# Optimization experiments

Measured on AMD Instinct MI355X. Metric: run time of the kernel, lower is better.

Reference implementation:

```python
import jax, jax.numpy as jnp
import numpy as np


def setup_inputs() -> dict:
    key = jax.random.key(0)
    ks = jax.random.split(key, 5)
    b, n_q, n_kv = 16, 128, 4096
    query_dim, context_dim, heads, dim_head = 1024, 1024, 16, 64
    inner = heads * dim_head
    x = jax.random.normal(ks[0], (b, n_q, query_dim), dtype=jnp.float32)
    context = jax.random.normal(ks[1], (b, n_kv, context_dim), dtype=jnp.float32)
    # Linear weights stored as (in, out); scaled like default torch init magnitude
    Wq = jax.random.normal(ks[2], (query_dim, inner), dtype=jnp.float32) * (query_dim ** -0.5)
    Wkv = jax.random.normal(ks[3], (context_dim, 2 * inner), dtype=jnp.float32) * (context_dim ** -0.5)
    Wout = jax.random.normal(ks[4], (inner, query_dim), dtype=jnp.float32) * (inner ** -0.5)
    bout = jnp.zeros((query_dim,), dtype=jnp.float32)
    return {"x": x, "context": context, "Wq": Wq, "Wkv": Wkv, "Wout": Wout, "bout": bout}


def reference(x, context, Wq, Wkv, Wout, bout):
    heads, dim_head = 16, 64
    b, n_q, _ = x.shape
    n_kv = context.shape[1]
    scale = dim_head ** -0.5

    q = x @ Wq                       # [b, n_q, h*d]
    kv = context @ Wkv               # [b, n_kv, 2*h*d]
    k, v = jnp.split(kv, 2, axis=-1)

    def split_heads(t):
        bb, n, _ = t.shape
        return t.reshape(bb, n, heads, dim_head).transpose(0, 2, 1, 3)  # [b, h, n, d]

    q, k, v = map(split_heads, (q, k, v))

    # mask[i, j] = (i - (j % n_q) == 0)  -> query i attends keys j with j % n_q == i
    i_idx = jnp.arange(n_q)[:, None]
    j_idx = jnp.arange(n_kv)[None, :]
    mask = (j_idx % n_q) == i_idx      # [n_q, n_kv] bool

    sim = jnp.einsum('bhid,bhjd->bhij', q, k) * scale
    max_neg = -jnp.finfo(sim.dtype).max
    sim = jnp.where(mask[None, None, :, :], sim, max_neg)
    attn = jax.nn.softmax(sim, axis=-1)
    out = jnp.einsum('bhij,bhjd->bhid', attn, v)   # [b, h, n_q, d]
    out = out.transpose(0, 2, 1, 3).reshape(b, n_q, heads * dim_head)
    return out @ Wout + bout
```

## Files before the change

### kernel.cpp

```cpp
#include <hip/hip_runtime.h>
#include <hip/hip_bf16.h>

typedef __attribute__((ext_vector_type(8))) short short8;
typedef __attribute__((ext_vector_type(4))) float floatx4;

__device__ __forceinline__ unsigned short f32_to_bf16(float f) {
    unsigned int u = __builtin_bit_cast(unsigned int, f);
    u = (u + 0x7FFFu + ((u >> 16) & 1u)) >> 16;
    return (unsigned short)u;
}
__device__ __forceinline__ unsigned int pack_bf16x2(float lo, float hi) {
    return (unsigned int)f32_to_bf16(lo) | ((unsigned int)f32_to_bf16(hi) << 16);
}
__device__ __forceinline__ void async_load16(const unsigned short* g, unsigned short* l) {
    __builtin_amdgcn_global_load_lds(
        (const __attribute__((address_space(1))) void*)g,
        (__attribute__((address_space(3))) void*)l, 16, 0, 0);
}

__device__ __forceinline__ void transpose_tile(
    const float* __restrict__ W, int src_ld, int n_off,
    unsigned short* __restrict__ Wt, int dst_ld, int nb, int kb, int tid) {
    __shared__ float tile[32][33];
    int n0 = nb * 32, k0 = kb * 32;
    int tx = tid & 31, ty = tid >> 5;
#pragma unroll
    for (int p = 0; p < 4; ++p) {
        int r = ty + 8 * p;
        tile[r][tx] = W[(long)(k0 + r) * src_ld + n_off + n0 + tx];
    }
    __syncthreads();
#pragma unroll
    for (int p = 0; p < 4; ++p) {
        int r = ty + 8 * p;
        Wt[(long)(n0 + r) * dst_ld + k0 + tx] = f32_to_bf16(tile[tx][r]);
    }
}

__device__ __forceinline__ void cast8(
    const float* __restrict__ src, unsigned short* __restrict__ dst) {
    float4 a = *(const float4*)src;
    float4 b = *(const float4*)(src + 4);
    uint4 p;
    p.x = pack_bf16x2(a.x, a.y); p.y = pack_bf16x2(a.z, a.w);
    p.z = pack_bf16x2(b.x, b.y); p.w = pack_bf16x2(b.z, b.w);
    *(uint4*)dst = p;
}

__global__ __launch_bounds__(256) void prep_kernel(
    const float* __restrict__ Wq, const float* __restrict__ Wkv,
    const float* __restrict__ Wout, const float* __restrict__ x,
    unsigned short* __restrict__ WqT, unsigned short* __restrict__ WkB,
    unsigned short* __restrict__ WvT, unsigned short* __restrict__ WoutT,
    unsigned short* __restrict__ xb) {
    int id = blockIdx.x, tid = threadIdx.x;
    if (id < 1024) { transpose_tile(Wq,   1024, 0,    WqT,   1024, id & 31, id >> 5, tid); return; }
    id -= 1024;
    if (id < 1024) { transpose_tile(Wkv,  2048, 1024, WvT,   1024, id & 31, id >> 5, tid); return; }
    id -= 1024;
    if (id < 1024) { transpose_tile(Wout, 1024, 0,    WoutT, 1024, id & 31, id >> 5, tid); return; }
    id -= 1024;
    if (id < 512) {
        long e = ((long)id * 256 + tid) * 8;
        long row = e >> 10, col = e & 1023;
        cast8(Wkv + row * 2048 + col, WkB + e);
        return;
    }
    id -= 512;
    { long e = ((long)id * 256 + tid) * 8; cast8(x + e, xb + e); }
}

__global__ __launch_bounds__(256, 2) void gemm_bt_kernel(
    const unsigned short* __restrict__ A, long sA, int lda,
    const unsigned short* __restrict__ Bt, long sB, int ldb,
    void* __restrict__ C, long sC, int ldc,
    const float* __restrict__ bias, int K, int out_bf16) {
    __shared__ unsigned short As[128 * 32];
    __shared__ unsigned short Bs[128 * 32];

    const int tid = threadIdx.x, wave = tid >> 6, lane = tid & 63;
    const int z = blockIdx.z;
    A  += (long)z * sA;
    Bt += (long)z * sB;
    const int m0 = blockIdx.y * 128, n0 = blockIdx.x * 128;
    const int wrow = (wave >> 1) * 64, wcol = (wave & 1) * 64;

    floatx4 acc[4][4];
#pragma unroll
    for (int i = 0; i < 4; ++i)
#pragma unroll
        for (int j = 0; j < 4; ++j) acc[i][j] = (floatx4)0.0f;

    const int srow = wave * 32 + (lane >> 2);
    const int kofs = (lane & 3) * 8;
    const unsigned short* aAddr = A  + (long)(m0 + srow) * lda + kofs;
    const unsigned short* bAddr = Bt + (long)(n0 + srow) * ldb + kofs;
    unsigned short* asBase = &As[wave * 1024];
    unsigned short* bsBase = &Bs[wave * 1024];

    const int frm = lane & 15, fk = (lane >> 4) * 8;

    for (int kk = 0; kk < K; kk += 32) {
        __syncthreads();
        async_load16(aAddr + kk,                  asBase);
        async_load16(aAddr + (long)16 * lda + kk, asBase + 512);
        async_load16(bAddr + kk,                  bsBase);
        async_load16(bAddr + (long)16 * ldb + kk, bsBase + 512);
        __syncthreads();

        short8 afrag[4], bfrag[4];
#pragma unroll
        for (int rt = 0; rt < 4; ++rt)
            afrag[rt] = *(const short8*)&As[(wrow + rt * 16 + frm) * 32 + fk];
#pragma unroll
        for (int ct = 0; ct < 4; ++ct)
            bfrag[ct] = *(const short8*)&Bs[(wcol + ct * 16 + frm) * 32 + fk];
#pragma unroll
        for (int rt = 0; rt < 4; ++rt)
#pragma unroll
            for (int ct = 0; ct < 4; ++ct)
                acc[rt][ct] = __builtin_amdgcn_mfma_f32_16x16x32_bf16(
                    afrag[rt], bfrag[ct], acc[rt][ct], 0, 0, 0);
    }

    const int orow0 = m0 + wrow + (lane >> 4) * 4;
    const int ocol0 = n0 + wcol + (lane & 15);
    if (out_bf16) {
        unsigned short* Cb = (unsigned short*)C + (long)z * sC;
#pragma unroll
        for (int rt = 0; rt < 4; ++rt)
#pragma unroll
            for (int r = 0; r < 4; ++r) {
                long row = orow0 + rt * 16 + r;
#pragma unroll
                for (int ct = 0; ct < 4; ++ct)
                    Cb[row * ldc + ocol0 + ct * 16] = f32_to_bf16(acc[rt][ct][r]);
            }
    } else {
        float* Cf = (float*)C + (long)z * sC;
#pragma unroll
        for (int rt = 0; rt < 4; ++rt)
#pragma unroll
            for (int r = 0; r < 4; ++r) {
                long row = orow0 + rt * 16 + r;
#pragma unroll
                for (int ct = 0; ct < 4; ++ct) {
                    int col = ocol0 + ct * 16;
                    float v = acc[rt][ct][r];
                    if (bias) v += bias[col];
                    Cf[row * ldc + col] = v;
                }
            }
    }
}

__global__ __launch_bounds__(256, 2) void gemm_n64_kernel(
    const unsigned short* __restrict__ A, long sA, int lda,
    const unsigned short* __restrict__ Bt, long sB, int ldb,
    unsigned short* __restrict__ C, long sC, int ldc, int K) {
    __shared__ unsigned short As[256 * 32];
    __shared__ unsigned short Bs[64 * 32];

    const int tid = threadIdx.x, wave = tid >> 6, lane = tid & 63;
    const int z = blockIdx.z;
    A  += (long)z * sA;
    Bt += (long)z * sB;
    C  += (long)z * sC;
    const int m0 = blockIdx.y * 256;

    floatx4 acc[4][4];
#pragma unroll
    for (int i = 0; i < 4; ++i)
#pragma unroll
        for (int j = 0; j < 4; ++j) acc[i][j] = (floatx4)0.0f;

    const int srow = tid >> 2;
    const int kofs = (tid & 3) * 8;
    const unsigned short* aBase = A  + (long)(m0 + srow) * lda + kofs;
    const unsigned short* bAddr = Bt + (long)srow * ldb + kofs;
    unsigned short* asW = &As[wave * 512];
    unsigned short* bsW = &Bs[wave * 512];

    const int frm = lane & 15, fk = (lane >> 4) * 8;

    for (int kk = 0; kk < K; kk += 32) {
        __syncthreads();
        async_load16(aBase + kk,                   asW);
        async_load16(aBase + (long)64  * lda + kk, asW + 2048);
        async_load16(aBase + (long)128 * lda + kk, asW + 4096);
        async_load16(aBase + (long)192 * lda + kk, asW + 6144);
        async_load16(bAddr + kk,                   bsW);
        __syncthreads();

        short8 afrag[4], bfrag[4];
#pragma unroll
        for (int rt = 0; rt < 4; ++rt)
            afrag[rt] = *(const short8*)&As[(wave * 64 + rt * 16 + frm) * 32 + fk];
#pragma unroll
        for (int ct = 0; ct < 4; ++ct)
            bfrag[ct] = *(const short8*)&Bs[(ct * 16 + frm) * 32 + fk];
#pragma unroll
        for (int rt = 0; rt < 4; ++rt)
#pragma unroll
            for (int ct = 0; ct < 4; ++ct)
                acc[rt][ct] = __builtin_amdgcn_mfma_f32_16x16x32_bf16(
                    afrag[rt], bfrag[ct], acc[rt][ct], 0, 0, 0);
    }

    const int orow0 = m0 + wave * 64 + (lane >> 4) * 4;
    const int ocol0 = lane & 15;
#pragma unroll
    for (int rt = 0; rt < 4; ++rt)
#pragma unroll
        for (int r = 0; r < 4; ++r) {
            long row = orow0 + rt * 16 + r;
#pragma unroll
            for (int ct = 0; ct < 4; ++ct)
                C[row * ldc + ocol0 + ct * 16] = f32_to_bf16(acc[rt][ct][r]);
        }
}

#define CLD 1032
__global__ __launch_bounds__(256) void attn_fused_kernel(
    const float* __restrict__ ctx,
    const unsigned short* __restrict__ qt,
    unsigned short* __restrict__ wctx) {
    __shared__ unsigned short ctx_t[32 * CLD];
    __shared__ unsigned short qt_t[16 * CLD];
    __shared__ float sred[4 * 512];
    __shared__ float s_f[512];
    __shared__ float mxs[16], inv_[16];
    __shared__ unsigned short p_l[16 * 40];

    const int tid = threadIdx.x, wave = tid >> 6, lane = tid & 63;
    const int bi = blockIdx.x;
    const int b = bi >> 7, i = bi & 127;
    const int frm = lane & 15, fk = (lane >> 4) * 8;

#pragma unroll
    for (int rr = 0; rr < 8; ++rr) {
        int idx = rr * 2048 + tid * 8;
        int h = idx >> 10, c = idx & 1023;
        *(uint4*)&qt_t[h * CLD + c] =
            *(const uint4*)&qt[(long)h * 2048 * 1024 + (long)bi * 1024 + c];
    }
#pragma unroll
    for (int rr = 0; rr < 16; ++rr) {
        int idx = rr * 2048 + tid * 8;
        int t = idx >> 10, c = idx & 1023;
        cast8(ctx + ((long)b * 4096 + i + t * 128) * 1024 + c, &ctx_t[t * CLD + c]);
    }
    __syncthreads();

    floatx4 acc0 = (floatx4)0.0f, acc1 = (floatx4)0.0f;
#pragma unroll
    for (int it = 0; it < 8; ++it) {
        int kk = wave * 256 + it * 32;
        short8 af = *(const short8*)&qt_t[frm * CLD + kk + fk];
        short8 b0 = *(const short8*)&ctx_t[frm * CLD + kk + fk];
        short8 b1 = *(const short8*)&ctx_t[(16 + frm) * CLD + kk + fk];
        acc0 = __builtin_amdgcn_mfma_f32_16x16x32_bf16(af, b0, acc0, 0, 0, 0);
        acc1 = __builtin_amdgcn_mfma_f32_16x16x32_bf16(af, b1, acc1, 0, 0, 0);
    }
#pragma unroll
    for (int r = 0; r < 4; ++r) {
        sred[wave * 512 + frm * 16 + (lane >> 4) * 4 + r]        = acc0[r];
        sred[wave * 512 + (16 + frm) * 16 + (lane >> 4) * 4 + r] = acc1[r];
    }
    __syncthreads();
#pragma unroll
    for (int half = 0; half < 2; ++half) {
        int idx = half * 256 + tid;
        s_f[idx] = (sred[idx] + sred[512 + idx] + sred[1024 + idx] + sred[1536 + idx]) * 0.125f;
    }
    __syncthreads();
    if (tid < 16) {
        int h = tid;
        float m = -1e30f;
        for (int t = 0; t < 32; ++t) m = fmaxf(m, s_f[t * 16 + h]);
        float den = 0.0f;
        for (int t = 0; t < 32; ++t) den += __expf(s_f[t * 16 + h] - m);
        mxs[h] = m; inv_[h] = 1.0f / den;
    }
    __syncthreads();
#pragma unroll
    for (int half = 0; half < 2; ++half) {
        int idx = half * 256 + tid;
        int t = idx >> 4, h = idx & 15;
        p_l[h * 40 + t] = f32_to_bf16(__expf(s_f[idx] - mxs[h]) * inv_[h]);
    }
    __syncthreads();

    short8 ap;
#pragma unroll
    for (int j = 0; j < 8; ++j) ap[j] = (short)p_l[frm * 40 + fk + j];
#pragma unroll 4
    for (int nt = 0; nt < 16; ++nt) {
        int c0 = wave * 256 + nt * 16;
        short8 bt;
#pragma unroll
        for (int j = 0; j < 8; ++j) bt[j] = (short)ctx_t[(fk + j) * CLD + c0 + frm];
        floatx4 wacc = __builtin_amdgcn_mfma_f32_16x16x32_bf16(ap, bt, (floatx4)0.0f, 0, 0, 0);
#pragma unroll
        for (int r = 0; r < 4; ++r) {
            int h = (lane >> 4) * 4 + r;
            wctx[(long)h * 2048 * 1024 + (long)bi * 1024 + c0 + frm] = f32_to_bf16(wacc[r]);
        }
    }
}

extern "C" void kernel_launch(void* const* d_in, const int* in_sizes, int n_in,
                              void* d_out, int out_size, void* d_ws, size_t ws_size,
                              hipStream_t stream) {
    const float* x       = (const float*)d_in[0];
    const float* context = (const float*)d_in[1];
    const float* Wq      = (const float*)d_in[2];
    const float* Wkv     = (const float*)d_in[3];
    const float* Wout    = (const float*)d_in[4];
    const float* bout    = (const float*)d_in[5];
    float* out = (float*)d_out;

    char* ws = (char*)d_ws;
    unsigned short* WqT   = (unsigned short*)(ws);
    unsigned short* WkB   = (unsigned short*)(ws + (2ll  << 20));
    unsigned short* WvT   = (unsigned short*)(ws + (4ll  << 20));
    unsigned short* WoutT = (unsigned short*)(ws + (6ll  << 20));
    unsigned short* xb    = (unsigned short*)(ws + (8ll  << 20));
    unsigned short* qb    = (unsigned short*)(ws + (12ll << 20));
    unsigned short* aob   = (unsigned short*)(ws + (16ll << 20));
    unsigned short* qtb   = (unsigned short*)(ws + (32ll << 20));
    unsigned short* wctxb = (unsigned short*)(ws + (96ll << 20));

    prep_kernel<<<4608, 256, 0, stream>>>(Wq, Wkv, Wout, x, WqT, WkB, WvT, WoutT, xb);

    gemm_bt_kernel<<<dim3(8, 16, 1), 256, 0, stream>>>(
        xb, 0, 1024, WqT, 0, 1024, qb, 0, 1024, nullptr, 1024, 1);
    gemm_bt_kernel<<<dim3(8, 16, 16), 256, 0, stream>>>(
        qb, 64, 1024, WkB, 64, 1024, qtb, (long)2048 * 1024, 1024, nullptr, 64, 1);
    attn_fused_kernel<<<2048, 256, 0, stream>>>(context, qtb, wctxb);
    gemm_n64_kernel<<<dim3(1, 8, 16), 256, 0, stream>>>(
        wctxb, (long)2048 * 1024, 1024, WvT, (long)64 * 1024, 1024, aob, 64, 1024, 1024);
    gemm_bt_kernel<<<dim3(8, 16, 1), 256, 0, stream>>>(
        aob, 0, 1024, WoutT, 0, 1024, out, 0, 1024, bout, 1024, 0);
}
```

Measured before the change: 501.1 us.

## Use one 128x64 GEMM kernel, batch-major qt/wctx layouts, register-resident Q in attention

Replaces the 128x128 and n64 GEMM kernels with a single 128x64-tile kernel that allows more blocks per CU, and launches twice as many blocks for the small GEMMs. The per-head intermediates qt and wctx move from head-major to batch-major layout so the attention kernel reads and writes contiguous 32KB per row. The attention kernel now loads its Q fragments straight into registers instead of staging them in LDS, which cuts LDS use and lets it declare two blocks per CU. The cost is smaller GEMM tiles with less operand reuse, and more global traffic for B tiles.

Result: faster. 478.9 us (-4.4%).

```diff
diff --git a/kernel.cpp b/kernel.cpp
--- a/kernel.cpp
+++ b/kernel.cpp
@@ -70,33 +70,31 @@
     { long e = ((long)id * 256 + tid) * 8; cast8(x + e, xb + e); }
 }
 
-__global__ __launch_bounds__(256, 2) void gemm_bt_kernel(
+__global__ __launch_bounds__(256, 4) void gemm64_kernel(
     const unsigned short* __restrict__ A, long sA, int lda,
     const unsigned short* __restrict__ Bt, long sB, int ldb,
     void* __restrict__ C, long sC, int ldc,
     const float* __restrict__ bias, int K, int out_bf16) {
     __shared__ unsigned short As[128 * 32];
-    __shared__ unsigned short Bs[128 * 32];
+    __shared__ unsigned short Bs[64 * 32];
 
     const int tid = threadIdx.x, wave = tid >> 6, lane = tid & 63;
     const int z = blockIdx.z;
     A  += (long)z * sA;
     Bt += (long)z * sB;
-    const int m0 = blockIdx.y * 128, n0 = blockIdx.x * 128;
-    const int wrow = (wave >> 1) * 64, wcol = (wave & 1) * 64;
-
-    floatx4 acc[4][4];
-#pragma unroll
-    for (int i = 0; i < 4; ++i)
+    const int m0 = blockIdx.y * 128, n0 = blockIdx.x * 64;
+
+    floatx4 acc[2][4];
+#pragma unroll
+    for (int i = 0; i < 2; ++i)
 #pragma unroll
         for (int j = 0; j < 4; ++j) acc[i][j] = (floatx4)0.0f;
 
-    const int srow = wave * 32 + (lane >> 2);
     const int kofs = (lane & 3) * 8;
-    const unsigned short* aAddr = A  + (long)(m0 + srow) * lda + kofs;
-    const unsigned short* bAddr = Bt + (long)(n0 + srow) * ldb + kofs;
+    const unsigned short* aAddr = A  + (long)(m0 + wave * 32 + (lane >> 2)) * lda + kofs;
+    const unsigned short* bAddr = Bt + (long)(n0 + wave * 16 + (lane >> 2)) * ldb + kofs;
     unsigned short* asBase = &As[wave * 1024];
-    unsigned short* bsBase = &Bs[wave * 1024];
+    unsigned short* bsBase = &Bs[wave * 512];
 
     const int frm = lane & 15, fk = (lane >> 4) * 8;
 
@@ -105,30 +103,29 @@
         async_load16(aAddr + kk,                  asBase);
         async_load16(aAddr + (long)16 * lda + kk, asBase + 512);
         async_load16(bAddr + kk,                  bsBase);
-        async_load16(bAddr + (long)16 * ldb + kk, bsBase + 512);
         __syncthreads();
 
-        short8 afrag[4], bfrag[4];
-#pragma unroll
-        for (int rt = 0; rt < 4; ++rt)
-            afrag[rt] = *(const short8*)&As[(wrow + rt * 16 + frm) * 32 + fk];
+        short8 afrag[2], bfrag[4];
+#pragma unroll
+        for (int rt = 0; rt < 2; ++rt)
+            afrag[rt] = *(const short8*)&As[(wave * 32 + rt * 16 + frm) * 32 + fk];
 #pragma unroll
         for (int ct = 0; ct < 4; ++ct)
-            bfrag[ct] = *(const short8*)&Bs[(wcol + ct * 16 + frm) * 32 + fk];
-#pragma unroll
-        for (int rt = 0; rt < 4; ++rt)
+            bfrag[ct] = *(const short8*)&Bs[(ct * 16 + frm) * 32 + fk];
+#pragma unroll
+        for (int rt = 0; rt < 2; ++rt)
 #pragma unroll
             for (int ct = 0; ct < 4; ++ct)
                 acc[rt][ct] = __builtin_amdgcn_mfma_f32_16x16x32_bf16(
                     afrag[rt], bfrag[ct], acc[rt][ct], 0, 0, 0);
     }
 
-    const int orow0 = m0 + wrow + (lane >> 4) * 4;
-    const int ocol0 = n0 + wcol + (lane & 15);
+    const int orow0 = m0 + wave * 32 + (lane >> 4) * 4;
+    const int ocol0 = n0 + (lane & 15);
     if (out_bf16) {
         unsigned short* Cb = (unsigned short*)C + (long)z * sC;
 #pragma unroll
-        for (int rt = 0; rt < 4; ++rt)
+        for (int rt = 0; rt < 2; ++rt)
 #pragma unroll
             for (int r = 0; r < 4; ++r) {
                 long row = orow0 + rt * 16 + r;
@@ -139,7 +136,7 @@
     } else {
         float* Cf = (float*)C + (long)z * sC;
 #pragma unroll
-        for (int rt = 0; rt < 4; ++rt)
+        for (int rt = 0; rt < 2; ++rt)
 #pragma unroll
             for (int r = 0; r < 4; ++r) {
                 long row = orow0 + rt * 16 + r;
@@ -154,79 +151,12 @@
     }
 }
 
-__global__ __launch_bounds__(256, 2) void gemm_n64_kernel(
-    const unsigned short* __restrict__ A, long sA, int lda,
-    const unsigned short* __restrict__ Bt, long sB, int ldb,
-    unsigned short* __restrict__ C, long sC, int ldc, int K) {
-    __shared__ unsigned short As[256 * 32];
-    __shared__ unsigned short Bs[64 * 32];
-
-    const int tid = threadIdx.x, wave = tid >> 6, lane = tid & 63;
-    const int z = blockIdx.z;
-    A  += (long)z * sA;
-    Bt += (long)z * sB;
-    C  += (long)z * sC;
-    const int m0 = blockIdx.y * 256;
-
-    floatx4 acc[4][4];
-#pragma unroll
-    for (int i = 0; i < 4; ++i)
-#pragma unroll
-        for (int j = 0; j < 4; ++j) acc[i][j] = (floatx4)0.0f;
-
-    const int srow = tid >> 2;
-    const int kofs = (tid & 3) * 8;
-    const unsigned short* aBase = A  + (long)(m0 + srow) * lda + kofs;
-    const unsigned short* bAddr = Bt + (long)srow * ldb + kofs;
-    unsigned short* asW = &As[wave * 512];
-    unsigned short* bsW = &Bs[wave * 512];
-
-    const int frm = lane & 15, fk = (lane >> 4) * 8;
-
-    for (int kk = 0; kk < K; kk += 32) {
-        __syncthreads();
-        async_load16(aBase + kk,                   asW);
-        async_load16(aBase + (long)64  * lda + kk, asW + 2048);
-        async_load16(aBase + (long)128 * lda + kk, asW + 4096);
-        async_load16(aBase + (long)192 * lda + kk, asW + 6144);
-        async_load16(bAddr + kk,                   bsW);
-        __syncthreads();
-
-        short8 afrag[4], bfrag[4];
-#pragma unroll
-        for (int rt = 0; rt < 4; ++rt)
-            afrag[rt] = *(const short8*)&As[(wave * 64 + rt * 16 + frm) * 32 + fk];
-#pragma unroll
-        for (int ct = 0; ct < 4; ++ct)
-            bfrag[ct] = *(const short8*)&Bs[(ct * 16 + frm) * 32 + fk];
-#pragma unroll
-        for (int rt = 0; rt < 4; ++rt)
-#pragma unroll
-            for (int ct = 0; ct < 4; ++ct)
-                acc[rt][ct] = __builtin_amdgcn_mfma_f32_16x16x32_bf16(
-                    afrag[rt], bfrag[ct], acc[rt][ct], 0, 0, 0);
-    }
-
-    const int orow0 = m0 + wave * 64 + (lane >> 4) * 4;
-    const int ocol0 = lane & 15;
-#pragma unroll
-    for (int rt = 0; rt < 4; ++rt)
-#pragma unroll
-        for (int r = 0; r < 4; ++r) {
-            long row = orow0 + rt * 16 + r;
-#pragma unroll
-            for (int ct = 0; ct < 4; ++ct)
-                C[row * ldc + ocol0 + ct * 16] = f32_to_bf16(acc[rt][ct][r]);
-        }
-}
-
 #define CLD 1032
-__global__ __launch_bounds__(256) void attn_fused_kernel(
+__global__ __launch_bounds__(256, 2) void attn_fused_kernel(
     const float* __restrict__ ctx,
     const unsigned short* __restrict__ qt,
     unsigned short* __restrict__ wctx) {
     __shared__ unsigned short ctx_t[32 * CLD];
-    __shared__ unsigned short qt_t[16 * CLD];
     __shared__ float sred[4 * 512];
     __shared__ float s_f[512];
     __shared__ float mxs[16], inv_[16];
@@ -237,13 +167,12 @@
     const int b = bi >> 7, i = bi & 127;
     const int frm = lane & 15, fk = (lane >> 4) * 8;
 
-#pragma unroll
-    for (int rr = 0; rr < 8; ++rr) {
-        int idx = rr * 2048 + tid * 8;
-        int h = idx >> 10, c = idx & 1023;
-        *(uint4*)&qt_t[h * CLD + c] =
-            *(const uint4*)&qt[(long)h * 2048 * 1024 + (long)bi * 1024 + c];
-    }
+    short8 af[8];
+    const unsigned short* qbase =
+        qt + (long)bi * 16384 + (long)frm * 1024 + wave * 256 + fk;
+#pragma unroll
+    for (int it = 0; it < 8; ++it) af[it] = *(const short8*)(qbase + it * 32);
+
 #pragma unroll
     for (int rr = 0; rr < 16; ++rr) {
         int idx = rr * 2048 + tid * 8;
@@ -256,11 +185,10 @@
 #pragma unroll
     for (int it = 0; it < 8; ++it) {
         int kk = wave * 256 + it * 32;
-        short8 af = *(const short8*)&qt_t[frm * CLD + kk + fk];
         short8 b0 = *(const short8*)&ctx_t[frm * CLD + kk + fk];
         short8 b1 = *(const short8*)&ctx_t[(16 + frm) * CLD + kk + fk];
-        acc0 = __builtin_amdgcn_mfma_f32_16x16x32_bf16(af, b0, acc0, 0, 0, 0);
-        acc1 = __builtin_amdgcn_mfma_f32_16x16x32_bf16(af, b1, acc1, 0, 0, 0);
+        acc0 = __builtin_amdgcn_mfma_f32_16x16x32_bf16(af[it], b0, acc0, 0, 0, 0);
+        acc1 = __builtin_amdgcn_mfma_f32_16x16x32_bf16(af[it], b1, acc1, 0, 0, 0);
     }
 #pragma unroll
     for (int r = 0; r < 4; ++r) {
@@ -304,7 +232,7 @@
 #pragma unroll
         for (int r = 0; r < 4; ++r) {
             int h = (lane >> 4) * 4 + r;
-            wctx[(long)h * 2048 * 1024 + (long)bi * 1024 + c0 + frm] = f32_to_bf16(wacc[r]);
+            wctx[(long)bi * 16384 + (long)h * 1024 + c0 + frm] = f32_to_bf16(wacc[r]);
         }
     }
 }
@@ -333,13 +261,13 @@
 
     prep_kernel<<<4608, 256, 0, stream>>>(Wq, Wkv, Wout, x, WqT, WkB, WvT, WoutT, xb);
 
-    gemm_bt_kernel<<<dim3(8, 16, 1), 256, 0, stream>>>(
+    gemm64_kernel<<<dim3(16, 16, 1), 256, 0, stream>>>(
         xb, 0, 1024, WqT, 0, 1024, qb, 0, 1024, nullptr, 1024, 1);
-    gemm_bt_kernel<<<dim3(8, 16, 16), 256, 0, stream>>>(
-        qb, 64, 1024, WkB, 64, 1024, qtb, (long)2048 * 1024, 1024, nullptr, 64, 1);
+    gemm64_kernel<<<dim3(16, 16, 16), 256, 0, stream>>>(
+        qb, 64, 1024, WkB, 64, 1024, qtb, 1024, 16384, nullptr, 64, 1);
     attn_fused_kernel<<<2048, 256, 0, stream>>>(context, qtb, wctxb);
-    gemm_n64_kernel<<<dim3(1, 8, 16), 256, 0, stream>>>(
-        wctxb, (long)2048 * 1024, 1024, WvT, (long)64 * 1024, 1024, aob, 64, 1024, 1024);
-    gemm_bt_kernel<<<dim3(8, 16, 1), 256, 0, stream>>>(
+    gemm64_kernel<<<dim3(1, 16, 16), 256, 0, stream>>>(
+        wctxb, 1024, 16384, WvT, (long)64 * 1024, 1024, aob, 64, 1024, nullptr, 1024, 1);
+    gemm64_kernel<<<dim3(16, 16, 1), 256, 0, stream>>>(
         aob, 0, 1024, WoutT, 0, 1024, out, 0, 1024, bout, 1024, 0);
 }
```
